# Kernel tuning notes

Measured on AMD Instinct MI355X. Metric: run time of the kernel, lower is better.

The kernel has to match this reference:

```python
import jax, jax.numpy as jnp
import numpy as np

HEADS = 8

def _ln(x, g, b):
    m = jnp.mean(x, -1, keepdims=True)
    v = jnp.mean((x - m) ** 2, -1, keepdims=True)
    return (x - m) * jax.lax.rsqrt(v + 1e-5) * g + b

def _l2n(t):
    n = jnp.sqrt(jnp.sum(t * t, -1, keepdims=True))
    return t / jnp.maximum(n, 1e-12)

def _xca(x, ln_g, ln_b, w_qkv, temp, w_out, b_out):
    B, H, W, D = x.shape
    n = H * W
    xf = x.reshape(B, n, D)
    h = _ln(xf, ln_g, ln_b)
    qkv = h @ w_qkv  # [B, n, 3*inner]
    q, k, v = jnp.split(qkv, 3, axis=-1)
    def tohd(t):
        return t.reshape(B, n, HEADS, -1).transpose(0, 2, 3, 1)  # b h d n
    q, k, v = tohd(q), tohd(k), tohd(v)
    q, k = _l2n(q), _l2n(k)
    sim = jnp.einsum('bhdn,bhen->bhde', q, k) * jnp.exp(temp)[None, :, None, None]
    attn = jax.nn.softmax(sim, axis=-1)
    out = jnp.einsum('bhde,bhen->bhdn', attn, v)
    out = out.transpose(0, 3, 1, 2).reshape(B, n, -1)  # b n (h d)
    return (out @ w_out + b_out).reshape(B, H, W, D)

def _dwconv(x, w, b):
    # x: [B,C,H,W], w: [C,1,k,k] depthwise
    y = jax.lax.conv_general_dilated(x, w, (1, 1), 'SAME',
                                     feature_group_count=x.shape[1],
                                     dimension_numbers=('NCHW', 'OIHW', 'NCHW'))
    return y + b[None, :, None, None]

def _lpi(x, ln_g, ln_b, w1, b1, bn_g, bn_b, w2, b2):
    h = _ln(x, ln_g, ln_b).transpose(0, 3, 1, 2)  # b c h w
    h = _dwconv(h, w1, b1)
    # BatchNorm2d (training-mode batch stats, biased var, eps=1e-5)
    m = jnp.mean(h, (0, 2, 3), keepdims=True)
    v = jnp.mean((h - m) ** 2, (0, 2, 3), keepdims=True)
    h = (h - m) * jax.lax.rsqrt(v + 1e-5) * bn_g[None, :, None, None] + bn_b[None, :, None, None]
    h = jax.nn.gelu(h, approximate=False)
    h = _dwconv(h, w2, b2)
    return h.transpose(0, 2, 3, 1)

def _ff(x, g, b, w1, b1, w2, b2):
    h = _ln(x, g, b)
    h = jax.nn.gelu(h @ w1 + b1, approximate=False)
    return h @ w2 + b2

def setup_inputs() -> dict:
    key = jax.random.key(0)
    D, depth, Hh, dh, M = 384, 4, 8, 48, 1536
    inner = Hh * dh
    B, H, W = 16, 48, 48
    ks = jax.random.split(key, 8)
    x = jax.random.normal(ks[0], (B, H, W, D), jnp.float32)
    def nrm(k, shape, s=0.02):
        return jax.random.normal(k, shape, jnp.float32) * s
    return dict(
        x=x,
        ln1_g=jnp.ones((depth, D)), ln1_b=jnp.zeros((depth, D)),
        w_qkv=nrm(ks[1], (depth, D, 3 * inner)),
        temp=jnp.ones((depth, Hh)),
        w_out=nrm(ks[2], (depth, inner, D)), b_out=jnp.zeros((depth, D)),
        scale_attn=jnp.full((depth, D), 0.1, jnp.float32),
        lpi_ln_g=jnp.ones((depth, D)), lpi_ln_b=jnp.zeros((depth, D)),
        conv1_w=nrm(ks[3], (depth, D, 1, 3, 3), 0.1), conv1_b=jnp.zeros((depth, D)),
        bn_g=jnp.ones((depth, D)), bn_b=jnp.zeros((depth, D)),
        conv2_w=nrm(ks[4], (depth, D, 1, 3, 3), 0.1), conv2_b=jnp.zeros((depth, D)),
        scale_lpi=jnp.full((depth, D), 0.1, jnp.float32),
        ff_ln_g=jnp.ones((depth, D)), ff_ln_b=jnp.zeros((depth, D)),
        w1=nrm(ks[5], (depth, D, M)), b1=jnp.zeros((depth, M)),
        w2=nrm(ks[6], (depth, M, D)), b2=jnp.zeros((depth, D)),
        scale_ff=jnp.full((depth, D), 0.1, jnp.float32),
    )

def reference(x, ln1_g, ln1_b, w_qkv, temp, w_out, b_out, scale_attn,
              lpi_ln_g, lpi_ln_b, conv1_w, conv1_b, bn_g, bn_b, conv2_w, conv2_b, scale_lpi,
              ff_ln_g, ff_ln_b, w1, b1, w2, b2, scale_ff):
    depth = ln1_g.shape[0]
    for i in range(depth):
        x = _xca(x, ln1_g[i], ln1_b[i], w_qkv[i], temp[i], w_out[i], b_out[i]) * scale_attn[i] + x
        x = _lpi(x, lpi_ln_g[i], lpi_ln_b[i], conv1_w[i], conv1_b[i], bn_g[i], bn_b[i], conv2_w[i], conv2_b[i]) * scale_lpi[i] + x
        x = _ff(x, ff_ln_g[i], ff_ln_b[i], w1[i], b1[i], w2[i], b2[i]) * scale_ff[i] + x
    return x
```

## Files before the change

kernel.cpp:

```cpp
#include <hip/hip_runtime.h>
#include <math.h>

typedef unsigned short u16;
typedef unsigned int   u32;
typedef u16   u16x8 __attribute__((ext_vector_type(8)));
typedef u16   u16x4 __attribute__((ext_vector_type(4)));
typedef short s16x8 __attribute__((ext_vector_type(8)));
typedef float f32x4 __attribute__((ext_vector_type(4)));

#define DEVFN static __device__ __forceinline__
#define GLOBAL_AS __attribute__((address_space(1)))
#define LDS_AS    __attribute__((address_space(3)))

constexpr int Bb = 16, Hh = 48, Ww = 48, Dd = 384;
constexpr int Nn = Hh * Ww;
constexpr int NT = Bb * Nn;
constexpr int NH = 8, DHd = 48;
constexpr int INNER = NH * DHd;
constexpr int QC = 3 * INNER;
constexpr int MF = 1536;
constexpr int DEPTH = 4;
constexpr int NCH = 6;

DEVFN float bf2f(u16 u) { return __uint_as_float(((u32)u) << 16); }
DEVFN u16   f2bu(float f) { u32 x = __float_as_uint(f); return (u16)((x + 0x7FFFu + ((x >> 16) & 1u)) >> 16); }
DEVFN float geluf(float x) { return 0.5f * x * (1.0f + erff(x * 0.70710678118654752440f)); }

DEVFN void gload16(const u16* g, u16* lds_base) {
    __builtin_amdgcn_global_load_lds((const GLOBAL_AS void*)g, (LDS_AS void*)lds_base, 16, 0, 0);
}

__global__ void k_copy(const float* __restrict__ in, float* __restrict__ X) {
    size_t i0 = ((size_t)blockIdx.x * 256 + threadIdx.x) * 4;
    *(f32x4*)(X + i0) = *(const f32x4*)(in + i0);
}

__global__ __launch_bounds__(256) void k_trb(const float* __restrict__ in, u16* __restrict__ out,
                                             int K, int N) {
    __shared__ float tile[64][65];
    in  += (size_t)blockIdx.z * K * N;
    out += (size_t)blockIdx.z * K * N;
    int k0 = blockIdx.y * 64, n0 = blockIdx.x * 64;
    int t = threadIdx.x;
    int r = t >> 4, c = (t & 15) * 4;
#pragma unroll
    for (int j = 0; j < 4; j++) {
        f32x4 v = *(const f32x4*)&in[(size_t)(k0 + r + j * 16) * N + n0 + c];
        tile[r + j * 16][c] = v[0]; tile[r + j * 16][c + 1] = v[1];
        tile[r + j * 16][c + 2] = v[2]; tile[r + j * 16][c + 3] = v[3];
    }
    __syncthreads();
#pragma unroll
    for (int j = 0; j < 4; j++) {
        u16x4 o;
#pragma unroll
        for (int i = 0; i < 4; i++) o[i] = f2bu(tile[c + i][r + j * 16]);
        *(u16x4*)&out[(size_t)(n0 + r + j * 16) * K + k0 + c] = o;
    }
}

__global__ __launch_bounds__(256) void k_ln(const float* __restrict__ X,
                                            const float* __restrict__ g, const float* __restrict__ bta,
                                            u16* __restrict__ out) {
    int row = blockIdx.x * 4 + (threadIdx.x >> 6);
    int lane = threadIdx.x & 63;
    const float* xr = X + (size_t)row * Dd;
    float v[6]; float s = 0.f, s2 = 0.f;
#pragma unroll
    for (int j = 0; j < 6; j++) { v[j] = xr[lane + 64 * j]; s += v[j]; s2 += v[j] * v[j]; }
#pragma unroll
    for (int off = 32; off >= 1; off >>= 1) { s += __shfl_down(s, off); s2 += __shfl_down(s2, off); }
    s = __shfl(s, 0); s2 = __shfl(s2, 0);
    float m = s * (1.0f / Dd);
    float rstd = 1.0f / sqrtf(s2 * (1.0f / Dd) - m * m + 1e-5f);
    u16* orow = out + (size_t)row * Dd;
#pragma unroll
    for (int j = 0; j < 6; j++) {
        int c = lane + 64 * j;
        orow[c] = f2bu((v[j] - m) * rstd * g[c] + bta[c]);
    }
}

__global__ __launch_bounds__(256) void k_lnstat(const float* __restrict__ X, float* __restrict__ LNS) {
    int row = blockIdx.x * 4 + (threadIdx.x >> 6);
    int lane = threadIdx.x & 63;
    const float* xr = X + (size_t)row * Dd;
    float s = 0.f, s2 = 0.f;
#pragma unroll
    for (int j = 0; j < 6; j++) { float v = xr[lane + 64 * j]; s += v; s2 += v * v; }
#pragma unroll
    for (int off = 32; off >= 1; off >>= 1) { s += __shfl_down(s, off); s2 += __shfl_down(s2, off); }
    if (lane == 0) {
        float m = s * (1.0f / Dd);
        float rstd = 1.0f / sqrtf(s2 * (1.0f / Dd) - m * m + 1e-5f);
        LNS[row * 2] = m;
        LNS[row * 2 + 1] = rstd;
    }
}

template <int MODE>
__global__ __launch_bounds__(512, 4) void k_mgemm(const u16* __restrict__ A, const u16* __restrict__ BT,
                                                  int Kdim, int Ndim,
                                                  const float* __restrict__ bias, const float* __restrict__ scale,
                                                  float* __restrict__ Xres, u16* __restrict__ Out,
                                                  float* __restrict__ QP) {
    __shared__ __align__(16) u16 Ts[3][24 * 512];
    __shared__ float QS[4][128];
    const int gridX = Ndim >> 7;
    const int nwg = gridX * (NT >> 8);
    const int cpx = nwg >> 3;
    const int id = blockIdx.x;
    const int id2 = (id & 7) * cpx + (id >> 3);
    const int n0 = (id2 % gridX) * 128;
    const int m0 = (id2 / gridX) * 256;
    const int t = threadIdx.x;
    const int w = t >> 6, l = t & 63;
    const int wm = w >> 1, wn = w & 1;
    const int lr = l >> 2;
    const int sc = ((l & 3) ^ (lr & 3)) * 8;
    const int fr = l & 15, rq = l >> 4;
    const int c0 = w * 3;

    auto stage = [&](int buf, int k0) {
#pragma unroll
        for (int j = 0; j < 3; j++) {
            const int c = c0 + j;
            const u16* src = (c < 16)
                ? A  + (size_t)(m0 + c * 16 + lr) * Kdim + k0 + sc
                : BT + (size_t)(n0 + (c - 16) * 16 + lr) * Kdim + k0 + sc;
            gload16(src, Ts[buf] + c * 512);
        }
    };

    const int nt = Kdim >> 5;
    stage(0, 0);
    stage(1, 32);

    f32x4 acc[4][4] = {};
    for (int kt = 0; kt < nt; ++kt) {
        if (kt + 1 < nt) {
            asm volatile("s_waitcnt vmcnt(3)" ::: "memory");
        } else {
            asm volatile("s_waitcnt vmcnt(0)" ::: "memory");
        }
        __builtin_amdgcn_s_barrier();
        __builtin_amdgcn_sched_barrier(0);
        if (kt + 2 < nt) stage((kt + 2) % 3, (kt + 2) * 32);
        const u16* ts = Ts[kt % 3];
        s16x8 af[4], bf[4];
#pragma unroll
        for (int f = 0; f < 4; f++) {
            const int row = wm * 64 + f * 16 + fr;
            af[f] = *(const s16x8*)&ts[row * 32 + ((rq ^ (fr & 3)) * 8)];
        }
#pragma unroll
        for (int g = 0; g < 4; g++) {
            const int row = wn * 64 + g * 16 + fr;
            bf[g] = *(const s16x8*)&ts[8192 + row * 32 + ((rq ^ (fr & 3)) * 8)];
        }
#pragma unroll
        for (int f = 0; f < 4; f++)
#pragma unroll
            for (int g = 0; g < 4; g++)
                acc[f][g] = __builtin_amdgcn_mfma_f32_16x16x32_bf16(af[f], bf[g], acc[f][g], 0, 0, 0);
    }

    float sq[4] = {0.f, 0.f, 0.f, 0.f};
#pragma unroll
    for (int g = 0; g < 4; g++) {
        const int n = n0 + wn * 64 + g * 16 + fr;
        float bv = (MODE == 1 || MODE == 2) ? bias[n] : 0.f;
        float sv = (MODE == 2) ? scale[n] : 0.f;
#pragma unroll
        for (int f = 0; f < 4; f++) {
            const size_t i0 = (size_t)(m0 + wm * 64 + f * 16 + rq * 4);
#pragma unroll
            for (int r = 0; r < 4; r++) {
                float v = acc[f][g][r];
                if (MODE == 0 || MODE == 3) {
                    Out[(i0 + r) * Ndim + n] = f2bu(v);
                    if (MODE == 3) sq[g] += v * v;
                } else if (MODE == 1) {
                    Out[(i0 + r) * Ndim + n] = f2bu(geluf(v + bv));
                } else {
                    float* xr = Xres + (i0 + r) * Ndim + n;
                    *xr += sv * (v + bv);
                }
            }
        }
    }

    if (MODE == 3 && n0 < 768) {
#pragma unroll
        for (int g = 0; g < 4; g++) {
            float s2 = sq[g];
            s2 += __shfl_down(s2, 32);
            s2 += __shfl_down(s2, 16);
            if (rq == 0) QS[wm][wn * 64 + g * 16 + fr] = s2;
        }
        __syncthreads();
        if (t < 128) {
            float s = QS[0][t] + QS[1][t] + QS[2][t] + QS[3][t];
            const int b_img = m0 / Nn, mset = (m0 % Nn) >> 8;
            QP[((size_t)(b_img * 9 + mset)) * 768 + n0 + t] = s;
        }
    }
}

__global__ void k_nrm_fin(const float* __restrict__ QP, float* __restrict__ INVN) {
    int idx = blockIdx.x * 256 + threadIdx.x;
    int b = idx / 768, c = idx - b * 768;
    float s = 0;
#pragma unroll
    for (int ms = 0; ms < 9; ms++) s += QP[((size_t)(b * 9 + ms)) * 768 + c];
    INVN[idx] = 1.0f / fmaxf(sqrtf(s), 1e-12f);
}

__global__ __launch_bounds__(256) void k_sim(const u16* __restrict__ QKV, float* __restrict__ SIMP) {
    const int bh = blockIdx.x;
    const int b = bh >> 3, h = bh & 7;
    const int chunk = blockIdx.y;
    __shared__ float qt[48][65];
    __shared__ float kt[48][65];
    const int t = threadIdx.x;
    const int w = t >> 6, l = t & 63;
    const int fr = l & 15, rq = l >> 4;
    const int ti0 = w, ti1 = w + 4;
    f32x4 acc0 = {}, acc1 = {}, acc2 = {};

    auto doTile = [&](int ti, f32x4& a) {
        const int d0 = (ti / 3) * 16, e0 = (ti % 3) * 16;
#pragma unroll
        for (int s = 0; s < 2; s++) {
            const float* qp = &qt[d0 + fr][s * 32 + rq * 8];
            const float* kp = &kt[e0 + fr][s * 32 + rq * 8];
            s16x8 af, bf;
#pragma unroll
            for (int j = 0; j < 8; j++) {
                af[j] = (short)(__float_as_uint(qp[j]) >> 16);
                bf[j] = (short)(__float_as_uint(kp[j]) >> 16);
            }
            a = __builtin_amdgcn_mfma_f32_16x16x32_bf16(af, bf, a, 0, 0, 0);
        }
    };

    for (int c0 = chunk * (Nn / NCH); c0 < (chunk + 1) * (Nn / NCH); c0 += 64) {
        __syncthreads();
        for (int e = t; e < 48 * 64; e += 256) {
            int r = e / 48, d = e - r * 48;
            const u16* p = QKV + (size_t)(b * Nn + c0 + r) * QC + h * DHd + d;
            qt[d][r] = bf2f(p[0]);
            kt[d][r] = bf2f(p[INNER]);
        }
        __syncthreads();
        doTile(ti0, acc0);
        doTile(ti1, acc1);
        if (w == 0) doTile(8, acc2);
    }

    float* so = SIMP + ((size_t)chunk * (Bb * NH) + bh) * (DHd * DHd);
    auto wr = [&](int ti, const f32x4& a) {
        const int d0 = (ti / 3) * 16, e0 = (ti % 3) * 16;
#pragma unroll
        for (int r = 0; r < 4; r++) so[(d0 + rq * 4 + r) * DHd + e0 + fr] = a[r];
    };
    wr(ti0, acc0);
    wr(ti1, acc1);
    if (w == 0) wr(8, acc2);
}

__global__ __launch_bounds__(256) void k_smax(const float* __restrict__ SIMP, float* __restrict__ SIM,
                                              const float* __restrict__ INVN, const float* __restrict__ temp) {
    int wid = blockIdx.x * 4 + (threadIdx.x >> 6);
    int lane = threadIdx.x & 63;
    int b = wid / (NH * DHd); int rem = wid - b * NH * DHd; int h = rem / DHd; int d = rem - h * DHd;
    int bh = b * NH + h;
    float et = expf(temp[h]);
    float invq = INVN[b * 768 + h * DHd + d];
    float myv = 0.f, mv = -3.0e38f;
    if (lane < DHd) {
        float s = 0.f;
#pragma unroll
        for (int c = 0; c < NCH; c++)
            s += SIMP[((size_t)c * (Bb * NH) + bh) * (DHd * DHd) + d * DHd + lane];
        myv = s * invq * INVN[b * 768 + 384 + h * DHd + lane] * et;
        mv = myv;
    }
#pragma unroll
    for (int off = 32; off >= 1; off >>= 1) mv = fmaxf(mv, __shfl_down(mv, off));
    mv = __shfl(mv, 0);
    float e = (lane < DHd) ? expf(myv - mv) : 0.f;
    float s = e;
#pragma unroll
    for (int off = 32; off >= 1; off >>= 1) s += __shfl_down(s, off);
    s = __shfl(s, 0);
    if (lane < DHd) SIM[(size_t)bh * (DHd * DHd) + d * DHd + lane] = e / s;
}

__global__ __launch_bounds__(256) void k_av(const u16* __restrict__ QKV, const float* __restrict__ SIM,
                                            u16* __restrict__ AOUT) {
    const int bh = blockIdx.x;
    const int b = bh >> 3, h = bh & 7;
    __shared__ __align__(16) float at[48][52];
    const int t = threadIdx.x;
    for (int e = t; e < 48 * 48; e += 256) at[e / 48][e % 48] = SIM[(size_t)bh * (DHd * DHd) + e];
    __syncthreads();
    const int r = blockIdx.y * 256 + t;
    const u16x8* vp = (const u16x8*)(QKV + (size_t)(b * Nn + r) * QC + 2 * INNER + h * DHd);
    f32x4 vv[12];
#pragma unroll
    for (int q8 = 0; q8 < 6; q8++) {
        u16x8 u = vp[q8];
#pragma unroll
        for (int j = 0; j < 8; j++) vv[q8 * 2 + (j >> 2)][j & 3] = bf2f(u[j]);
    }
    u16x8 ob[6];
#pragma unroll
    for (int d = 0; d < 48; d++) {
        f32x4 sv = {0.f, 0.f, 0.f, 0.f};
#pragma unroll
        for (int e4 = 0; e4 < 12; e4++) sv += *(const f32x4*)&at[d][e4 * 4] * vv[e4];
        ob[d >> 3][d & 7] = f2bu(sv[0] + sv[1] + sv[2] + sv[3]);
    }
    u16x8* orow = (u16x8*)(AOUT + (size_t)(b * Nn + r) * Dd + h * DHd);
#pragma unroll
    for (int q8 = 0; q8 < 6; q8++) orow[q8] = ob[q8];
}

__global__ __launch_bounds__(384) void k_lpi1(const float* __restrict__ X, const float* __restrict__ LNS,
                                              const float* __restrict__ g, const float* __restrict__ bta,
                                              const float* __restrict__ wgt, const float* __restrict__ cbias,
                                              u16* __restrict__ CF, float* __restrict__ BNP) {
    const int c = threadIdx.x;
    const int by = blockIdx.x;
    const int y = by % Hh, b = by / Hh;
    const int x0 = blockIdx.y * (Ww / 2);
    float w9[9];
#pragma unroll
    for (int j = 0; j < 9; j++) w9[j] = wgt[c * 9 + j];
    const float gc = g[c], bc = bta[c], cb = cbias[c];
    const size_t base = (size_t)b * Nn * Dd;
    const float* lns = LNS + (size_t)b * Nn * 2;

    auto load3 = [&](int xx, float* col) {
        if (xx < 0 || xx >= Ww) { col[0] = col[1] = col[2] = 0.f; return; }
#pragma unroll
        for (int dy = 0; dy < 3; dy++) {
            int yy = y + dy - 1;
            if (yy < 0 || yy >= Hh) { col[dy] = 0.f; }
            else {
                int tok = yy * Ww + xx;
                float m = lns[tok * 2], r = lns[tok * 2 + 1];
                col[dy] = (X[base + (size_t)tok * Dd + c] - m) * r * gc + bc;
            }
        }
    };

    float A[3], B[3], C[3], T[3];
    load3(x0 - 1, A); load3(x0, B); load3(x0 + 1, C);
    float s = 0.f, s2 = 0.f;
    u16* crow = CF + base + ((size_t)y * Ww + x0) * Dd + c;
    for (int x = x0; x < x0 + Ww / 2; x++) {
        load3(x + 2, T);
        float acc = cb;
#pragma unroll
        for (int dy = 0; dy < 3; dy++)
            acc += w9[dy * 3] * A[dy] + w9[dy * 3 + 1] * B[dy] + w9[dy * 3 + 2] * C[dy];
        crow[(size_t)(x - x0) * Dd] = f2bu(acc);
        s += acc; s2 += acc * acc;
#pragma unroll
        for (int dy = 0; dy < 3; dy++) { A[dy] = B[dy]; B[dy] = C[dy]; C[dy] = T[dy]; }
    }
    float* o = BNP + ((size_t)by * 2 + blockIdx.y) * 768;
    o[c] = s; o[384 + c] = s2;
}

__global__ __launch_bounds__(384) void k_bnred1(const float* __restrict__ BNP, float* __restrict__ BNQ) {
    int t = threadIdx.x, blk = blockIdx.x;
    float s = 0.f, s2 = 0.f;
    for (int i = blk * 24; i < blk * 24 + 24; i++) { s += BNP[(size_t)i * 768 + t]; s2 += BNP[(size_t)i * 768 + 384 + t]; }
    BNQ[(size_t)blk * 768 + t] = s; BNQ[(size_t)blk * 768 + 384 + t] = s2;
}

__global__ __launch_bounds__(384) void k_bnred2(const float* __restrict__ BNQ,
                                                const float* __restrict__ bng, const float* __restrict__ bnb,
                                                float* __restrict__ BNC) {
    int t = threadIdx.x;
    float s = 0.f, s2 = 0.f;
    for (int i = 0; i < 64; i++) { s += BNQ[(size_t)i * 768 + t]; s2 += BNQ[(size_t)i * 768 + 384 + t]; }
    float m = s / NT;
    float var = s2 / NT - m * m;
    float r = 1.0f / sqrtf(var + 1e-5f);
    BNC[t] = r * bng[t];
    BNC[384 + t] = bnb[t] - m * r * bng[t];
}

__global__ __launch_bounds__(384) void k_lpi2(const u16* __restrict__ CF, const float* __restrict__ BNC,
                                              const float* __restrict__ wgt, const float* __restrict__ cbias,
                                              const float* __restrict__ scale, float* __restrict__ X,
                                              const float* __restrict__ ffg, const float* __restrict__ ffb,
                                              u16* __restrict__ Hb) {
    __shared__ float XS[24][388];
    __shared__ float MS[24][2];
    const int c = threadIdx.x;
    const int by = blockIdx.x;
    const int y = by % Hh, b = by / Hh;
    const int x0 = blockIdx.y * (Ww / 2);
    float w9[9];
#pragma unroll
    for (int j = 0; j < 9; j++) w9[j] = wgt[c * 9 + j];
    const float bnA = BNC[c], bnB = BNC[384 + c];
    const float cb = cbias[c], sc = scale[c];
    const size_t base = (size_t)b * Nn * Dd;

    auto load3 = [&](int xx, float* col) {
        if (xx < 0 || xx >= Ww) { col[0] = col[1] = col[2] = 0.f; return; }
#pragma unroll
        for (int dy = 0; dy < 3; dy++) {
            int yy = y + dy - 1;
            if (yy < 0 || yy >= Hh) { col[dy] = 0.f; }
            else {
                int tok = yy * Ww + xx;
                col[dy] = geluf(bf2f(CF[base + (size_t)tok * Dd + c]) * bnA + bnB);
            }
        }
    };

    float A[3], B[3], C[3], T[3];
    load3(x0 - 1, A); load3(x0, B); load3(x0 + 1, C);
    float* xrow = X + base + ((size_t)y * Ww + x0) * Dd + c;
    for (int x = x0; x < x0 + Ww / 2; x++) {
        load3(x + 2, T);
        float acc = cb;
#pragma unroll
        for (int dy = 0; dy < 3; dy++)
            acc += w9[dy * 3] * A[dy] + w9[dy * 3 + 1] * B[dy] + w9[dy * 3 + 2] * C[dy];
        float xnew = xrow[(size_t)(x - x0) * Dd] + sc * acc;
        xrow[(size_t)(x - x0) * Dd] = xnew;
        XS[x - x0][c] = xnew;
#pragma unroll
        for (int dy = 0; dy < 3; dy++) { A[dy] = B[dy]; B[dy] = C[dy]; C[dy] = T[dy]; }
    }
    __syncthreads();

    const int wv = c >> 6, lane = c & 63;
#pragma unroll
    for (int k = 0; k < 4; k++) {
        const int tt = wv * 4 + k;
        float s = 0.f, s2 = 0.f;
#pragma unroll
        for (int j = 0; j < 6; j++) { float v = XS[tt][lane + 64 * j]; s += v; s2 += v * v; }
#pragma unroll
        for (int off = 32; off >= 1; off >>= 1) { s += __shfl_down(s, off); s2 += __shfl_down(s2, off); }
        if (lane == 0) {
            float m = s * (1.0f / Dd);
            MS[tt][0] = m;
            MS[tt][1] = 1.0f / sqrtf(s2 * (1.0f / Dd) - m * m + 1e-5f);
        }
    }
    __syncthreads();

    const float gc = ffg[c], bc2 = ffb[c];
    u16* hrow = Hb + base + ((size_t)y * Ww + x0) * Dd + c;
#pragma unroll 4
    for (int x = 0; x < 24; x++) {
        float h = (XS[x][c] - MS[x][0]) * MS[x][1] * gc + bc2;
        hrow[(size_t)x * Dd] = f2bu(h);
    }
}

extern "C" void kernel_launch(void* const* d_in, const int* in_sizes, int n_in,
                              void* d_out, int out_size, void* d_ws, size_t ws_size,
                              hipStream_t stream) {
    const float* x     = (const float*)d_in[0];
    const float* ln1_g = (const float*)d_in[1];
    const float* ln1_b = (const float*)d_in[2];
    const float* w_qkv = (const float*)d_in[3];
    const float* temp  = (const float*)d_in[4];
    const float* w_out = (const float*)d_in[5];
    const float* b_out = (const float*)d_in[6];
    const float* s_att = (const float*)d_in[7];
    const float* lpi_g = (const float*)d_in[8];
    const float* lpi_b = (const float*)d_in[9];
    const float* c1w   = (const float*)d_in[10];
    const float* c1b   = (const float*)d_in[11];
    const float* bng   = (const float*)d_in[12];
    const float* bnb   = (const float*)d_in[13];
    const float* c2w   = (const float*)d_in[14];
    const float* c2b   = (const float*)d_in[15];
    const float* s_lpi = (const float*)d_in[16];
    const float* ff_g  = (const float*)d_in[17];
    const float* ff_b  = (const float*)d_in[18];
    const float* w1    = (const float*)d_in[19];
    const float* b1    = (const float*)d_in[20];
    const float* w2    = (const float*)d_in[21];
    const float* b2    = (const float*)d_in[22];
    const float* s_ff  = (const float*)d_in[23];

    float* X = (float*)d_out;

    char* p = (char*)d_ws;
    auto carve = [&](size_t bytes) -> char* { char* r = p; p += (bytes + 255) / 256 * 256; return r; };
    u16*   BIG  = (u16*)  carve((size_t)NT * MF * 2);
    u16*   Hb   = (u16*)  carve((size_t)NT * Dd * 2);
    float* SIM  = (float*)carve((size_t)Bb * NH * DHd * DHd * 4);
    float* SIMP = (float*)carve((size_t)NCH * Bb * NH * DHd * DHd * 4);
    float* INVN = (float*)carve((size_t)Bb * 768 * 4);
    float* QP   = (float*)carve((size_t)Bb * 9 * 768 * 4);
    float* LNS  = (float*)carve((size_t)NT * 2 * 4);
    float* BNP  = (float*)carve((size_t)1536 * 768 * 4);
    float* BNQ  = (float*)carve((size_t)64 * 768 * 4);
    float* BNC  = (float*)carve((size_t)768 * 4);
    u16*   WQT  = (u16*)  carve((size_t)DEPTH * Dd * QC * 2);
    u16*   WOT  = (u16*)  carve((size_t)DEPTH * INNER * Dd * 2);
    u16*   W1T  = (u16*)  carve((size_t)DEPTH * Dd * MF * 2);
    u16*   W2T  = (u16*)  carve((size_t)DEPTH * MF * Dd * 2);
    u16*   AO   = BIG + (size_t)NT * QC;
    u16*   CF   = BIG;

    k_trb<<<dim3(QC / 64, Dd / 64, DEPTH), 256, 0, stream>>>(w_qkv, WQT, Dd, QC);
    k_trb<<<dim3(Dd / 64, INNER / 64, DEPTH), 256, 0, stream>>>(w_out, WOT, INNER, Dd);
    k_trb<<<dim3(MF / 64, Dd / 64, DEPTH), 256, 0, stream>>>(w1, W1T, Dd, MF);
    k_trb<<<dim3(Dd / 64, MF / 64, DEPTH), 256, 0, stream>>>(w2, W2T, MF, Dd);

    k_copy<<<NT * Dd / 1024, 256, 0, stream>>>(x, X);
    for (int L = 0; L < DEPTH; L++) {
        k_ln<<<NT / 4, 256, 0, stream>>>(X, ln1_g + L * Dd, ln1_b + L * Dd, Hb);
        k_mgemm<3><<<(QC / 128) * (NT / 256), 512, 0, stream>>>(Hb, WQT + (size_t)L * Dd * QC, Dd, QC,
                                                                nullptr, nullptr, nullptr, BIG, QP);
        k_nrm_fin<<<Bb * 768 / 256, 256, 0, stream>>>(QP, INVN);
        k_sim<<<dim3(Bb * NH, NCH), 256, 0, stream>>>(BIG, SIMP);
        k_smax<<<Bb * NH * DHd / 4, 256, 0, stream>>>(SIMP, SIM, INVN, temp + L * NH);
        k_av<<<dim3(Bb * NH, Nn / 256), 256, 0, stream>>>(BIG, SIM, AO);
        k_mgemm<2><<<(Dd / 128) * (NT / 256), 512, 0, stream>>>(AO, WOT + (size_t)L * INNER * Dd, INNER, Dd,
                                                                b_out + L * Dd, s_att + L * Dd, X, nullptr, nullptr);
        k_lnstat<<<NT / 4, 256, 0, stream>>>(X, LNS);
        k_lpi1<<<dim3(Bb * Hh, 2), 384, 0, stream>>>(X, LNS, lpi_g + L * Dd, lpi_b + L * Dd,
                                                     c1w + (size_t)L * Dd * 9, c1b + L * Dd, CF, BNP);
        k_bnred1<<<64, 384, 0, stream>>>(BNP, BNQ);
        k_bnred2<<<1, 384, 0, stream>>>(BNQ, bng + L * Dd, bnb + L * Dd, BNC);
        k_lpi2<<<dim3(Bb * Hh, 2), 384, 0, stream>>>(CF, BNC, c2w + (size_t)L * Dd * 9, c2b + L * Dd,
                                                     s_lpi + L * Dd, X, ff_g + L * Dd, ff_b + L * Dd, Hb);
        k_mgemm<1><<<(MF / 128) * (NT / 256), 512, 0, stream>>>(Hb, W1T + (size_t)L * Dd * MF, Dd, MF,
                                                                b1 + L * MF, nullptr, nullptr, BIG, nullptr);
        k_mgemm<2><<<(Dd / 128) * (NT / 256), 512, 0, stream>>>(BIG, W2T + (size_t)L * MF * Dd, MF, Dd,
                                                                b2 + L * Dd, s_ff + L * Dd, X, nullptr, nullptr);
    }
}
```

Before: 2.138 ms.

## Fuse LN row stats into out-proj GEMM epilogue; move FF LN out of lpi2

Adds a GEMM epilogue mode that, after the residual update, accumulates per-row sum and sum-of-squares and writes partial stats per column tile. A small finalize kernel combines the three partials into mean/rstd, which replaces the separate full-row stats pass over X. The feed-forward LayerNorm that was fused into k_lpi2 is split back out into a standalone k_ln launch, so k_lpi2 loses its shared-memory tile and two barriers but X is read once more. The epilogue adds LDS reduction work and extra registers to the GEMM.

```diff
diff --git a/kernel.cpp b/kernel.cpp
--- a/kernel.cpp
+++ b/kernel.cpp
@@ -78,23 +78,6 @@
     for (int j = 0; j < 6; j++) {
         int c = lane + 64 * j;
         orow[c] = f2bu((v[j] - m) * rstd * g[c] + bta[c]);
-    }
-}
-
-__global__ __launch_bounds__(256) void k_lnstat(const float* __restrict__ X, float* __restrict__ LNS) {
-    int row = blockIdx.x * 4 + (threadIdx.x >> 6);
-    int lane = threadIdx.x & 63;
-    const float* xr = X + (size_t)row * Dd;
-    float s = 0.f, s2 = 0.f;
-#pragma unroll
-    for (int j = 0; j < 6; j++) { float v = xr[lane + 64 * j]; s += v; s2 += v * v; }
-#pragma unroll
-    for (int off = 32; off >= 1; off >>= 1) { s += __shfl_down(s, off); s2 += __shfl_down(s2, off); }
-    if (lane == 0) {
-        float m = s * (1.0f / Dd);
-        float rstd = 1.0f / sqrtf(s2 * (1.0f / Dd) - m * m + 1e-5f);
-        LNS[row * 2] = m;
-        LNS[row * 2 + 1] = rstd;
     }
 }
 
@@ -166,11 +149,18 @@
     }
 
     float sq[4] = {0.f, 0.f, 0.f, 0.f};
+    float rs[4][4], rs2[4][4];
+    if (MODE == 4) {
+#pragma unroll
+        for (int f = 0; f < 4; f++)
+#pragma unroll
+            for (int r = 0; r < 4; r++) { rs[f][r] = 0.f; rs2[f][r] = 0.f; }
+    }
 #pragma unroll
     for (int g = 0; g < 4; g++) {
         const int n = n0 + wn * 64 + g * 16 + fr;
-        float bv = (MODE == 1 || MODE == 2) ? bias[n] : 0.f;
-        float sv = (MODE == 2) ? scale[n] : 0.f;
+        float bv = (MODE == 1 || MODE == 2 || MODE == 4) ? bias[n] : 0.f;
+        float sv = (MODE == 2 || MODE == 4) ? scale[n] : 0.f;
 #pragma unroll
         for (int f = 0; f < 4; f++) {
             const size_t i0 = (size_t)(m0 + wm * 64 + f * 16 + rq * 4);
@@ -184,7 +174,9 @@
                     Out[(i0 + r) * Ndim + n] = f2bu(geluf(v + bv));
                 } else {
                     float* xr = Xres + (i0 + r) * Ndim + n;
-                    *xr += sv * (v + bv);
+                    float xnew = *xr + sv * (v + bv);
+                    *xr = xnew;
+                    if (MODE == 4) { rs[f][r] += xnew; rs2[f][r] += xnew * xnew; }
                 }
             }
         }
@@ -205,6 +197,28 @@
             QP[((size_t)(b_img * 9 + mset)) * 768 + n0 + t] = s;
         }
     }
+
+    if (MODE == 4) {
+        __syncthreads();
+        float* S = (float*)&Ts[0][0];
+        const int col = wn * 16 + fr;
+#pragma unroll
+        for (int f = 0; f < 4; f++)
+#pragma unroll
+            for (int r = 0; r < 4; r++) {
+                const int row = wm * 64 + f * 16 + rq * 4 + r;
+                S[row * 32 + col] = rs[f][r];
+                S[8192 + row * 32 + col] = rs2[f][r];
+            }
+        __syncthreads();
+        const int row = t & 255;
+        const int comp = t >> 8;
+        const float* Sb = S + comp * 8192 + row * 32;
+        float s = 0.f;
+#pragma unroll
+        for (int i = 0; i < 32; i++) s += Sb[i];
+        QP[(((size_t)(n0 >> 7)) * NT + (m0 + row)) * 2 + comp] = s;
+    }
 }
 
 __global__ void k_nrm_fin(const float* __restrict__ QP, float* __restrict__ INVN) {
@@ -214,6 +228,16 @@
 #pragma unroll
     for (int ms = 0; ms < 9; ms++) s += QP[((size_t)(b * 9 + ms)) * 768 + c];
     INVN[idx] = 1.0f / fmaxf(sqrtf(s), 1e-12f);
+}
+
+__global__ void k_lnfin(const float* __restrict__ LNP, float* __restrict__ LNS) {
+    int row = blockIdx.x * 256 + threadIdx.x;
+    float s  = LNP[((size_t)0 * NT + row) * 2]     + LNP[((size_t)1 * NT + row) * 2]     + LNP[((size_t)2 * NT + row) * 2];
+    float s2 = LNP[((size_t)0 * NT + row) * 2 + 1] + LNP[((size_t)1 * NT + row) * 2 + 1] + LNP[((size_t)2 * NT + row) * 2 + 1];
+    float m = s * (1.0f / Dd);
+    float rstd = 1.0f / sqrtf(s2 * (1.0f / Dd) - m * m + 1e-5f);
+    LNS[row * 2] = m;
+    LNS[row * 2 + 1] = rstd;
 }
 
 __global__ __launch_bounds__(256) void k_sim(const u16* __restrict__ QKV, float* __restrict__ SIMP) {
@@ -397,11 +421,7 @@
 
 __global__ __launch_bounds__(384) void k_lpi2(const u16* __restrict__ CF, const float* __restrict__ BNC,
                                               const float* __restrict__ wgt, const float* __restrict__ cbias,
-                                              const float* __restrict__ scale, float* __restrict__ X,
-                                              const float* __restrict__ ffg, const float* __restrict__ ffb,
-                                              u16* __restrict__ Hb) {
-    __shared__ float XS[24][388];
-    __shared__ float MS[24][2];
+                                              const float* __restrict__ scale, float* __restrict__ X) {
     const int c = threadIdx.x;
     const int by = blockIdx.x;
     const int y = by % Hh, b = by / Hh;
@@ -435,37 +455,9 @@
 #pragma unroll
         for (int dy = 0; dy < 3; dy++)
             acc += w9[dy * 3] * A[dy] + w9[dy * 3 + 1] * B[dy] + w9[dy * 3 + 2] * C[dy];
-        float xnew = xrow[(size_t)(x - x0) * Dd] + sc * acc;
-        xrow[(size_t)(x - x0) * Dd] = xnew;
-        XS[x - x0][c] = xnew;
+        xrow[(size_t)(x - x0) * Dd] += sc * acc;
 #pragma unroll
         for (int dy = 0; dy < 3; dy++) { A[dy] = B[dy]; B[dy] = C[dy]; C[dy] = T[dy]; }
-    }
-    __syncthreads();
-
-    const int wv = c >> 6, lane = c & 63;
-#pragma unroll
-    for (int k = 0; k < 4; k++) {
-        const int tt = wv * 4 + k;
-        float s = 0.f, s2 = 0.f;
-#pragma unroll
-        for (int j = 0; j < 6; j++) { float v = XS[tt][lane + 64 * j]; s += v; s2 += v * v; }
-#pragma unroll
-        for (int off = 32; off >= 1; off >>= 1) { s += __shfl_down(s, off); s2 += __shfl_down(s2, off); }
-        if (lane == 0) {
-            float m = s * (1.0f / Dd);
-            MS[tt][0] = m;
-            MS[tt][1] = 1.0f / sqrtf(s2 * (1.0f / Dd) - m * m + 1e-5f);
-        }
-    }
-    __syncthreads();
-
-    const float gc = ffg[c], bc2 = ffb[c];
-    u16* hrow = Hb + base + ((size_t)y * Ww + x0) * Dd + c;
-#pragma unroll 4
-    for (int x = 0; x < 24; x++) {
-        float h = (XS[x][c] - MS[x][0]) * MS[x][1] * gc + bc2;
-        hrow[(size_t)x * Dd] = f2bu(h);
     }
 }
 
@@ -507,6 +499,7 @@
     float* SIMP = (float*)carve((size_t)NCH * Bb * NH * DHd * DHd * 4);
     float* INVN = (float*)carve((size_t)Bb * 768 * 4);
     float* QP   = (float*)carve((size_t)Bb * 9 * 768 * 4);
+    float* LNP  = (float*)carve((size_t)3 * NT * 2 * 4);
     float* LNS  = (float*)carve((size_t)NT * 2 * 4);
     float* BNP  = (float*)carve((size_t)1536 * 768 * 4);
     float* BNQ  = (float*)carve((size_t)64 * 768 * 4);
@@ -532,15 +525,16 @@
         k_sim<<<dim3(Bb * NH, NCH), 256, 0, stream>>>(BIG, SIMP);
         k_smax<<<Bb * NH * DHd / 4, 256, 0, stream>>>(SIMP, SIM, INVN, temp + L * NH);
         k_av<<<dim3(Bb * NH, Nn / 256), 256, 0, stream>>>(BIG, SIM, AO);
-        k_mgemm<2><<<(Dd / 128) * (NT / 256), 512, 0, stream>>>(AO, WOT + (size_t)L * INNER * Dd, INNER, Dd,
-                                                                b_out + L * Dd, s_att + L * Dd, X, nullptr, nullptr);
-        k_lnstat<<<NT / 4, 256, 0, stream>>>(X, LNS);
+        k_mgemm<4><<<(Dd / 128) * (NT / 256), 512, 0, stream>>>(AO, WOT + (size_t)L * INNER * Dd, INNER, Dd,
+                                                                b_out + L * Dd, s_att + L * Dd, X, nullptr, LNP);
+        k_lnfin<<<NT / 256, 256, 0, stream>>>(LNP, LNS);
         k_lpi1<<<dim3(Bb * Hh, 2), 384, 0, stream>>>(X, LNS, lpi_g + L * Dd, lpi_b + L * Dd,
                                                      c1w + (size_t)L * Dd * 9, c1b + L * Dd, CF, BNP);
         k_bnred1<<<64, 384, 0, stream>>>(BNP, BNQ);
         k_bnred2<<<1, 384, 0, stream>>>(BNQ, bng + L * Dd, bnb + L * Dd, BNC);
         k_lpi2<<<dim3(Bb * Hh, 2), 384, 0, stream>>>(CF, BNC, c2w + (size_t)L * Dd * 9, c2b + L * Dd,
-                                                     s_lpi + L * Dd, X, ff_g + L * Dd, ff_b + L * Dd, Hb);
+                                                     s_lpi + L * Dd, X);
+        k_ln<<<NT / 4, 256, 0, stream>>>(X, ff_g + L * Dd, ff_b + L * Dd, Hb);
         k_mgemm<1><<<(MF / 128) * (NT / 256), 512, 0, stream>>>(Hb, W1T + (size_t)L * Dd * MF, Dd, MF,
                                                                 b1 + L * MF, nullptr, nullptr, BIG, nullptr);
         k_mgemm<2><<<(Dd / 128) * (NT / 256), 512, 0, stream>>>(BIG, W2T + (size_t)L * MF * Dd, MF, Dd,
```

Measured after the change: 1.989 ms (median of 2 runs). 1.08x faster.
